# Performance work log

Hardware: AMD Instinct MI355X
Metric: run time of the kernel (lower is better)

Reference implementation:

```python
import jax, jax.numpy as jnp
import numpy as np

LOG2 = float(np.log(2.0))

def shifted_softplus(x):
    return jax.nn.softplus(x) - LOG2

def setup_inputs() -> dict:
    key = jax.random.key(0)
    ks = jax.random.split(key, 12)
    N, E = 100000, 1600000
    Cin, Cout, F_, G = 128, 128, 128, 50
    x = jax.random.normal(ks[0], (N, Cin), dtype=jnp.float32)
    edge_index = jax.random.randint(ks[1], (2, E), 0, N, dtype=jnp.int64)
    edge_attr = jax.random.uniform(ks[2], (E, G), dtype=jnp.float32)
    s = lambda fan_in: 1.0 / np.sqrt(fan_in)
    lin1_w = jax.random.uniform(ks[3], (F_, Cin), jnp.float32, -s(Cin), s(Cin))
    lin1_b = jax.random.uniform(ks[4], (F_,), jnp.float32, -s(Cin), s(Cin))
    lin2_w = jax.random.uniform(ks[5], (Cout, F_), jnp.float32, -s(F_), s(F_))
    lin2_b = jax.random.uniform(ks[6], (Cout,), jnp.float32, -s(F_), s(F_))
    fn1_w = jax.random.uniform(ks[7], (F_, G), jnp.float32, -s(G), s(G))
    fn1_b = jax.random.uniform(ks[8], (F_,), jnp.float32, -s(G), s(G))
    fn2_w = jax.random.uniform(ks[9], (F_, F_), jnp.float32, -s(F_), s(F_))
    fn2_b = jax.random.uniform(ks[10], (F_,), jnp.float32, -s(F_), s(F_))
    return {"x": x, "edge_index": edge_index, "edge_attr": edge_attr,
            "lin1_w": lin1_w, "lin1_b": lin1_b, "lin2_w": lin2_w, "lin2_b": lin2_b,
            "fn1_w": fn1_w, "fn1_b": fn1_b, "fn2_w": fn2_w, "fn2_b": fn2_b}

def reference(x, edge_index, edge_attr, lin1_w, lin1_b, lin2_w, lin2_b,
              fn1_w, fn1_b, fn2_w, fn2_b):
    row, col = edge_index[0], edge_index[1]
    # filter network: [E, G] -> [E, F]
    W = shifted_softplus(edge_attr @ fn1_w.T + fn1_b) @ fn2_w.T + fn2_b
    # transform nodes then gather source features: [E, F]
    x_j = (x @ lin1_w.T + lin1_b)[col]
    msg = x_j * W
    # scatter-add over destination nodes: [N, F]
    agg = jax.ops.segment_sum(msg, row, num_segments=x.shape[0])
    return agg @ lin2_w.T + lin2_b
```

## Files before the change

### kernel.cpp

```cpp
#include <hip/hip_runtime.h>

#define NN 100000
#define NE 1600000
#define CC 128
#define GG 50
#define EPB 128

typedef _Float16 half8 __attribute__((ext_vector_type(8)));
typedef float f32x4 __attribute__((ext_vector_type(4)));

static __device__ __forceinline__ f32x4 mfma16(half8 a, half8 b, f32x4 c) {
    return __builtin_amdgcn_mfma_f32_16x16x32_f16(a, b, c, 0, 0, 0);
}

__global__ __launch_bounds__(256) void pack_frags(const float* fn1_w, const float* fn2_w,
                                                  _Float16* ws_frag)
{
    int tid = threadIdx.x;
    for (int s = tid; s < 1024; s += 256) {
        int l = s & 63, ks = (s >> 6) & 1, nb = s >> 7;
        int f = nb * 16 + (l & 15);
        int k0 = ks * 32 + 8 * (l >> 4);
        half8 v;
        #pragma unroll
        for (int i = 0; i < 8; i++) {
            int g = k0 + i;
            v[i] = (g < GG) ? (_Float16)fn1_w[f * GG + g] : (_Float16)0.f;
        }
        *reinterpret_cast<half8*>(&ws_frag[s * 8]) = v;
    }
    for (int s = tid; s < 2048; s += 256) {
        int l = s & 63, ks = (s >> 6) & 3, nb = s >> 8;
        int f = nb * 16 + (l & 15);
        int k0 = ks * 32 + 8 * (l >> 4);
        const float* wp = fn2_w + f * CC + k0;
        half8 v;
        #pragma unroll
        for (int i = 0; i < 8; i++) v[i] = (_Float16)wp[i];
        *reinterpret_cast<half8*>(&ws_frag[8192 + s * 8]) = v;
    }
}

template <typename OutT>
__global__ __launch_bounds__(256) void lin_kernel(const float* in, const float* w,
                                                  const float* bias, OutT* out, int nrows)
{
    __shared__ __align__(16) _Float16 a_lds[64][136];
    __shared__ __align__(16) _Float16 bfrag[2048 * 8];

    int tid = threadIdx.x;
    int rowBase = blockIdx.x * 64;

    for (int i = tid; i < 64 * 32; i += 256) {
        int r = i >> 5, c4 = i & 31;
        float4 v = {0.f, 0.f, 0.f, 0.f};
        if (rowBase + r < nrows)
            v = reinterpret_cast<const float4*>(in)[(size_t)(rowBase + r) * (CC / 4) + c4];
        a_lds[r][c4 * 4 + 0] = (_Float16)v.x;
        a_lds[r][c4 * 4 + 1] = (_Float16)v.y;
        a_lds[r][c4 * 4 + 2] = (_Float16)v.z;
        a_lds[r][c4 * 4 + 3] = (_Float16)v.w;
    }
    for (int s = tid; s < 2048; s += 256) {
        int l = s & 63, ks = (s >> 6) & 3, nb = s >> 8;
        int f = nb * 16 + (l & 15);
        int k0 = ks * 32 + 8 * (l >> 4);
        const float* wp = w + f * CC + k0;
        half8 v;
        #pragma unroll
        for (int i = 0; i < 8; i++) v[i] = (_Float16)wp[i];
        *reinterpret_cast<half8*>(&bfrag[s * 8]) = v;
    }
    __syncthreads();

    int wid = tid >> 6, l = tid & 63;
    int lr = l & 15, lg = l >> 4;
    int wrow = wid * 16;

    half8 afr[4];
    #pragma unroll
    for (int ks = 0; ks < 4; ks++)
        afr[ks] = *reinterpret_cast<const half8*>(&a_lds[wrow + lr][ks * 32 + 8 * lg]);

    #pragma unroll
    for (int nb = 0; nb < 8; nb++) {
        f32x4 acc = {0.f, 0.f, 0.f, 0.f};
        #pragma unroll
        for (int ks = 0; ks < 4; ks++) {
            half8 bf = *reinterpret_cast<const half8*>(&bfrag[((nb * 4 + ks) * 64 + l) * 8]);
            acc = mfma16(afr[ks], bf, acc);
        }
        float bv = bias[nb * 16 + lr];
        #pragma unroll
        for (int j = 0; j < 4; j++) {
            int r = rowBase + wrow + lg * 4 + j;
            if (r < nrows) out[(size_t)r * CC + nb * 16 + lr] = (OutT)(acc[j] + bv);
        }
    }
}

__global__ __launch_bounds__(512, 8) void edge_kernel(
    const _Float16* __restrict__ x1, const int* __restrict__ eidx,
    const float* __restrict__ ea, const _Float16* __restrict__ frag_ws,
    const float* __restrict__ fn1_b, const float* __restrict__ fn2_b,
    float* __restrict__ agg)
{
    __shared__ __align__(16) unsigned char u_lds[EPB * CC * 2];
    __shared__ int rows_l[EPB];
    __shared__ int cols_l[EPB];

    int tid = threadIdx.x;
    size_t eBase = (size_t)blockIdx.x * EPB;

    if (tid < EPB) {
        rows_l[tid] = eidx[eBase + tid];
        cols_l[tid] = eidx[(size_t)NE + eBase + tid];
    }

    {
        const float2* eap = reinterpret_cast<const float2*>(ea + eBase * GG);
        for (int i = tid; i < EPB * 25; i += 512) {
            int e = i / 25, g2 = i - e * 25;
            float2 v = eap[i];
            int byte = e * 128 + ((g2 * 4) ^ ((e & 7) << 4));
            _Float16* p = reinterpret_cast<_Float16*>(u_lds + byte);
            p[0] = (_Float16)v.x;
            p[1] = (_Float16)v.y;
        }
        for (int i = tid; i < EPB * 14; i += 512) {
            int e = i / 14, g = (i - e * 14) + 50;
            int byte = e * 128 + ((g * 2) ^ ((e & 7) << 4));
            *reinterpret_cast<_Float16*>(u_lds + byte) = (_Float16)0.f;
        }
    }
    __syncthreads();

    int w = tid >> 6, l = tid & 63;
    int lr = l & 15, lg = l >> 4;
    int erow = w * 16;

    half8 a1[2];
    #pragma unroll
    for (int ks = 0; ks < 2; ks++) {
        int e = erow + lr;
        int byte = e * 128 + ((ks * 64 + lg * 16) ^ ((e & 7) << 4));
        a1[ks] = *reinterpret_cast<const half8*>(u_lds + byte);
    }

    __syncthreads();

    #pragma unroll
    for (int nb = 0; nb < 8; nb++) {
        half8 b10 = *reinterpret_cast<const half8*>(&frag_ws[((nb * 2 + 0) * 64 + l) * 8]);
        half8 b11 = *reinterpret_cast<const half8*>(&frag_ws[((nb * 2 + 1) * 64 + l) * 8]);
        f32x4 acc = {0.f, 0.f, 0.f, 0.f};
        acc = mfma16(a1[0], b10, acc);
        acc = mfma16(a1[1], b11, acc);
        float bv = fn1_b[nb * 16 + lr];
        int f = nb * 16 + lr;
        #pragma unroll
        for (int j = 0; j < 4; j++) {
            float z = acc[j] + bv;
            float t = __expf(-fabsf(z));
            float h = fmaxf(z, 0.f) + __logf(1.f + t) - 0.69314718055994531f;
            int e = erow + lg * 4 + j;
            int byte = e * 256 + ((f * 2) ^ ((e & 7) << 4));
            *reinterpret_cast<_Float16*>(u_lds + byte) = (_Float16)h;
        }
    }
    __syncthreads();

    half8 a2[4];
    #pragma unroll
    for (int ks = 0; ks < 4; ks++) {
        int e = erow + lr;
        int byte = e * 256 + ((ks * 64 + lg * 16) ^ ((e & 7) << 4));
        a2[ks] = *reinterpret_cast<const half8*>(u_lds + byte);
    }

    int rr[4], cc4[4];
    #pragma unroll
    for (int j = 0; j < 4; j++) {
        int e = erow + lg * 4 + j;
        rr[j] = rows_l[e];
        cc4[j] = cols_l[e];
    }

    const half8* b2g = reinterpret_cast<const half8*>(frag_ws + 8192);
    #pragma unroll
    for (int nb = 0; nb < 8; nb++) {
        f32x4 acc = {0.f, 0.f, 0.f, 0.f};
        #pragma unroll
        for (int ks = 0; ks < 4; ks++) {
            half8 bf = b2g[(nb * 4 + ks) * 64 + l];
            acc = mfma16(a2[ks], bf, acc);
        }
        float bv = fn2_b[nb * 16 + lr];
        int f = nb * 16 + lr;
        #pragma unroll
        for (int j = 0; j < 4; j++) {
            float wv = acc[j] + bv;
            float xv = (float)x1[(size_t)cc4[j] * CC + f];
            atomicAdd(&agg[(size_t)rr[j] * CC + f], xv * wv);
        }
    }
}

extern "C" void kernel_launch(void* const* d_in, const int* in_sizes, int n_in,
                              void* d_out, int out_size, void* d_ws, size_t ws_size,
                              hipStream_t stream) {
    const float* x      = (const float*)d_in[0];
    const int*   eidx   = (const int*)d_in[1];
    const float* ea     = (const float*)d_in[2];
    const float* lin1_w = (const float*)d_in[3];
    const float* lin1_b = (const float*)d_in[4];
    const float* lin2_w = (const float*)d_in[5];
    const float* lin2_b = (const float*)d_in[6];
    const float* fn1_w  = (const float*)d_in[7];
    const float* fn1_b  = (const float*)d_in[8];
    const float* fn2_w  = (const float*)d_in[9];
    const float* fn2_b  = (const float*)d_in[10];

    float* out = (float*)d_out;
    _Float16* frag_ws = (_Float16*)d_ws;
    _Float16* x1h = (_Float16*)((char*)d_ws + 65536);
    float* agg = out;

    hipMemsetAsync(agg, 0, (size_t)NN * CC * sizeof(float), stream);

    pack_frags<<<1, 256, 0, stream>>>(fn1_w, fn2_w, frag_ws);
    lin_kernel<_Float16><<<(NN + 63) / 64, 256, 0, stream>>>(x, lin1_w, lin1_b, x1h, NN);
    edge_kernel<<<NE / EPB, 512, 0, stream>>>(x1h, eidx, ea, frag_ws, fn1_b, fn2_b, agg);
    lin_kernel<float><<<(NN + 63) / 64, 256, 0, stream>>>(agg, lin2_w, lin2_b, out, NN);
}
```

Measured before the change: 788.0 us.

## Sort edges by destination via counting sort and pre-reduce messages before atomics

Builds a per-call counting sort of edges by destination row (histogram, three-stage scan, permutation build). The edge kernel then processes edges in sorted order and does segmented reductions over runs of equal rows in LDS before issuing atomics. The aim is fewer global float atomics, since each 32-edge chunk holds only about two edges per destination on average. In exchange, edge_attr and col gathers become random-access through the permutation, there are several extra kernel launches and extra atomic passes for sorting, and messages are rounded to fp16 before summation. It falls back to the old atomic kernel if the workspace is too small.

```diff
diff --git a/kernel.cpp b/kernel.cpp
--- a/kernel.cpp
+++ b/kernel.cpp
@@ -5,6 +5,7 @@
 #define CC 128
 #define GG 50
 #define EPB 128
+#define NSCB 98
 
 typedef _Float16 half8 __attribute__((ext_vector_type(8)));
 typedef float f32x4 __attribute__((ext_vector_type(4)));
@@ -99,7 +100,210 @@
     }
 }
 
-__global__ __launch_bounds__(512, 8) void edge_kernel(
+__global__ __launch_bounds__(256) void hist_kernel(const int* row, int* cnt) {
+    int e = blockIdx.x * 256 + threadIdx.x;
+    if (e < NE) atomicAdd(&cnt[row[e]], 1);
+}
+
+__global__ __launch_bounds__(256) void scanA(const int* cnt, int* excl, int* bsum) {
+    __shared__ int lds[256];
+    int b = blockIdx.x, t = threadIdx.x;
+    int base = b * 1024 + t * 4;
+    int v[4];
+    #pragma unroll
+    for (int i = 0; i < 4; i++) v[i] = (base + i < NN) ? cnt[base + i] : 0;
+    int s = v[0] + v[1] + v[2] + v[3];
+    lds[t] = s;
+    __syncthreads();
+    for (int off = 1; off < 256; off <<= 1) {
+        int x = (t >= off) ? lds[t - off] : 0;
+        __syncthreads();
+        lds[t] += x;
+        __syncthreads();
+    }
+    int incl = lds[t];
+    int run = incl - s;
+    #pragma unroll
+    for (int i = 0; i < 4; i++) {
+        if (base + i < NN) excl[base + i] = run;
+        run += v[i];
+    }
+    if (t == 255) bsum[b] = incl;
+}
+
+__global__ __launch_bounds__(128) void scanB(int* bsum) {
+    __shared__ int lds[128];
+    int t = threadIdx.x;
+    int v = (t < NSCB) ? bsum[t] : 0;
+    lds[t] = v;
+    __syncthreads();
+    for (int off = 1; off < 128; off <<= 1) {
+        int x = (t >= off) ? lds[t - off] : 0;
+        __syncthreads();
+        lds[t] += x;
+        __syncthreads();
+    }
+    if (t < NSCB) bsum[t] = lds[t] - v;
+}
+
+__global__ __launch_bounds__(256) void scanC(int* excl, const int* bsum) {
+    int b = blockIdx.x, t = threadIdx.x;
+    int off = bsum[b];
+    int base = b * 1024 + t * 4;
+    #pragma unroll
+    for (int i = 0; i < 4; i++)
+        if (base + i < NN) excl[base + i] += off;
+}
+
+__global__ __launch_bounds__(256) void build_perm(const int* row, int* cursor, int* perm) {
+    int e = blockIdx.x * 256 + threadIdx.x;
+    if (e < NE) {
+        int r = row[e];
+        int p = atomicAdd(&cursor[r], 1);
+        perm[p] = e;
+    }
+}
+
+__global__ __launch_bounds__(512, 8) void edge_kernel_sorted(
+    const _Float16* __restrict__ x1, const int* __restrict__ eidx,
+    const float* __restrict__ ea, const _Float16* __restrict__ frag_ws,
+    const float* __restrict__ fn1_b, const float* __restrict__ fn2_b,
+    const int* __restrict__ perm, float* __restrict__ agg)
+{
+    __shared__ __align__(16) unsigned char u_lds[EPB * CC * 2];
+    __shared__ int pe_l[EPB];
+    __shared__ int row_l[EPB];
+    __shared__ int col_l[EPB];
+
+    int tid = threadIdx.x;
+    size_t eBase = (size_t)blockIdx.x * EPB;
+
+    if (tid < EPB) pe_l[tid] = perm[eBase + tid];
+    __syncthreads();
+
+    if (tid < EPB) {
+        int pe = pe_l[tid];
+        row_l[tid] = eidx[pe];
+        col_l[tid] = eidx[(size_t)NE + pe];
+    }
+    {
+        int i = tid >> 2, p = tid & 3;
+        int pe = pe_l[i];
+        const float2* src = reinterpret_cast<const float2*>(ea + (size_t)pe * GG);
+        int swz = (i & 7) << 4;
+        #pragma unroll
+        for (int it = 0; it < 7; it++) {
+            int g2 = p + it * 4;
+            if (g2 < 25) {
+                float2 v = src[g2];
+                int byte = i * 128 + ((g2 * 4) ^ swz);
+                _Float16* q = reinterpret_cast<_Float16*>(u_lds + byte);
+                q[0] = (_Float16)v.x;
+                q[1] = (_Float16)v.y;
+            }
+        }
+        #pragma unroll
+        for (int it = 0; it < 2; it++) {
+            int g2 = 25 + p + it * 4;
+            if (g2 < 32) {
+                int byte = i * 128 + ((g2 * 4) ^ swz);
+                _Float16* q = reinterpret_cast<_Float16*>(u_lds + byte);
+                q[0] = (_Float16)0.f;
+                q[1] = (_Float16)0.f;
+            }
+        }
+    }
+    __syncthreads();
+
+    int w = tid >> 6, l = tid & 63;
+    int lr = l & 15, lg = l >> 4;
+    int erow = w * 16;
+
+    half8 a1[2];
+    #pragma unroll
+    for (int ks = 0; ks < 2; ks++) {
+        int e = erow + lr;
+        int byte = e * 128 + ((ks * 64 + lg * 16) ^ ((e & 7) << 4));
+        a1[ks] = *reinterpret_cast<const half8*>(u_lds + byte);
+    }
+    __syncthreads();
+
+    #pragma unroll
+    for (int nb = 0; nb < 8; nb++) {
+        half8 b10 = *reinterpret_cast<const half8*>(&frag_ws[((nb * 2 + 0) * 64 + l) * 8]);
+        half8 b11 = *reinterpret_cast<const half8*>(&frag_ws[((nb * 2 + 1) * 64 + l) * 8]);
+        f32x4 acc = {0.f, 0.f, 0.f, 0.f};
+        acc = mfma16(a1[0], b10, acc);
+        acc = mfma16(a1[1], b11, acc);
+        float bv = fn1_b[nb * 16 + lr];
+        int f = nb * 16 + lr;
+        #pragma unroll
+        for (int j = 0; j < 4; j++) {
+            float z = acc[j] + bv;
+            float t = __expf(-fabsf(z));
+            float h = fmaxf(z, 0.f) + __logf(1.f + t) - 0.69314718055994531f;
+            int e = erow + lg * 4 + j;
+            int byte = e * 256 + ((f * 2) ^ ((e & 7) << 4));
+            *reinterpret_cast<_Float16*>(u_lds + byte) = (_Float16)h;
+        }
+    }
+    __syncthreads();
+
+    half8 a2[4];
+    #pragma unroll
+    for (int ks = 0; ks < 4; ks++) {
+        int e = erow + lr;
+        int byte = e * 256 + ((ks * 64 + lg * 16) ^ ((e & 7) << 4));
+        a2[ks] = *reinterpret_cast<const half8*>(u_lds + byte);
+    }
+
+    int cc4[4];
+    #pragma unroll
+    for (int j = 0; j < 4; j++) cc4[j] = col_l[erow + lg * 4 + j];
+
+    const half8* b2g = reinterpret_cast<const half8*>(frag_ws + 8192);
+    #pragma unroll
+    for (int nb = 0; nb < 8; nb++) {
+        f32x4 acc = {0.f, 0.f, 0.f, 0.f};
+        #pragma unroll
+        for (int ks = 0; ks < 4; ks++) {
+            half8 bf = b2g[(nb * 4 + ks) * 64 + l];
+            acc = mfma16(a2[ks], bf, acc);
+        }
+        float bv = fn2_b[nb * 16 + lr];
+        int f = nb * 16 + lr;
+        #pragma unroll
+        for (int j = 0; j < 4; j++) {
+            int e = erow + lg * 4 + j;
+            float wv = acc[j] + bv;
+            float xv = (float)x1[(size_t)cc4[j] * CC + f];
+            int byte = e * 256 + ((f * 2) ^ ((e & 7) << 4));
+            *reinterpret_cast<_Float16*>(u_lds + byte) = (_Float16)(xv * wv);
+        }
+    }
+    __syncthreads();
+
+    {
+        int f = tid & 127;
+        int c0 = (tid >> 7) * 32;
+        float acc = 0.f;
+        int cur = row_l[c0];
+        for (int k = 0; k < 32; k++) {
+            int e = c0 + k;
+            int r = row_l[e];
+            if (r != cur) {
+                atomicAdd(&agg[(size_t)cur * CC + f], acc);
+                acc = 0.f;
+                cur = r;
+            }
+            int byte = e * 256 + ((f * 2) ^ ((e & 7) << 4));
+            acc += (float)*reinterpret_cast<const _Float16*>(u_lds + byte);
+        }
+        atomicAdd(&agg[(size_t)cur * CC + f], acc);
+    }
+}
+
+__global__ __launch_bounds__(512, 8) void edge_kernel_atomic(
     const _Float16* __restrict__ x1, const int* __restrict__ eidx,
     const float* __restrict__ ea, const _Float16* __restrict__ frag_ws,
     const float* __restrict__ fn1_b, const float* __restrict__ fn2_b,
@@ -116,7 +320,6 @@
         rows_l[tid] = eidx[eBase + tid];
         cols_l[tid] = eidx[(size_t)NE + eBase + tid];
     }
-
     {
         const float2* eap = reinterpret_cast<const float2*>(ea + eBase * GG);
         for (int i = tid; i < EPB * 25; i += 512) {
@@ -146,7 +349,6 @@
         int byte = e * 128 + ((ks * 64 + lg * 16) ^ ((e & 7) << 4));
         a1[ks] = *reinterpret_cast<const half8*>(u_lds + byte);
     }
-
     __syncthreads();
 
     #pragma unroll
@@ -222,14 +424,42 @@
     const float* fn2_b  = (const float*)d_in[10];
 
     float* out = (float*)d_out;
-    _Float16* frag_ws = (_Float16*)d_ws;
-    _Float16* x1h = (_Float16*)((char*)d_ws + 65536);
     float* agg = out;
 
+    const size_t o_frag   = 0;
+    const size_t o_x1h    = 65536;
+    const size_t o_perm   = o_x1h + (size_t)NN * CC * 2;
+    const size_t o_rowptr = o_perm + (size_t)NE * 4;
+    const size_t o_bsum   = o_rowptr + (size_t)(NN + 1) * 4 + 60;
+    const size_t o_cnt    = o_bsum + 1024;
+    const size_t req      = o_cnt + (size_t)NN * 4;
+
+    _Float16* frag_ws = (_Float16*)((char*)d_ws + o_frag);
+    _Float16* x1h     = (_Float16*)((char*)d_ws + o_x1h);
+
     hipMemsetAsync(agg, 0, (size_t)NN * CC * sizeof(float), stream);
-
     pack_frags<<<1, 256, 0, stream>>>(fn1_w, fn2_w, frag_ws);
     lin_kernel<_Float16><<<(NN + 63) / 64, 256, 0, stream>>>(x, lin1_w, lin1_b, x1h, NN);
-    edge_kernel<<<NE / EPB, 512, 0, stream>>>(x1h, eidx, ea, frag_ws, fn1_b, fn2_b, agg);
+
+    if (ws_size >= req) {
+        int* perm   = (int*)((char*)d_ws + o_perm);
+        int* rowptr = (int*)((char*)d_ws + o_rowptr);
+        int* bsum   = (int*)((char*)d_ws + o_bsum);
+        int* cnt    = (int*)((char*)d_ws + o_cnt);
+
+        hipMemsetAsync(cnt, 0, (size_t)NN * 4, stream);
+        hist_kernel<<<(NE + 255) / 256, 256, 0, stream>>>(eidx, cnt);
+        scanA<<<NSCB, 256, 0, stream>>>(cnt, rowptr, bsum);
+        scanB<<<1, 128, 0, stream>>>(bsum);
+        scanC<<<NSCB, 256, 0, stream>>>(rowptr, bsum);
+        build_perm<<<(NE + 255) / 256, 256, 0, stream>>>(eidx, rowptr, perm);
+
+        edge_kernel_sorted<<<NE / EPB, 512, 0, stream>>>(x1h, eidx, ea, frag_ws,
+                                                         fn1_b, fn2_b, perm, agg);
+    } else {
+        edge_kernel_atomic<<<NE / EPB, 512, 0, stream>>>(x1h, eidx, ea, frag_ws,
+                                                         fn1_b, fn2_b, agg);
+    }
+
     lin_kernel<float><<<(NN + 63) / 64, 256, 0, stream>>>(agg, lin2_w, lin2_b, out, NN);
 }
```

Result: no change. 784.7 us (-0.4%).
